# Kernel tuning notes

Measured on AMD Instinct MI355X. Metric: run time of the kernel, lower is better.

## Reference

```python
import jax, jax.numpy as jnp
import numpy as np
import math

N_HEAD = 16
ROPE_BASE = 10000.0


def _rope_cos_sin(seq_len, head_dim, dtype):
    # standard RoPE tables: freqs_i = base^(-2i/d), i in [0, d/2)
    half = head_dim // 2
    inv_freq = ROPE_BASE ** (-(jnp.arange(half, dtype=jnp.float32) * 2.0 / head_dim))
    t = jnp.arange(seq_len, dtype=jnp.float32)
    ang = t[:, None] * inv_freq[None, :]  # [S, d/2]
    return jnp.cos(ang).astype(dtype), jnp.sin(ang).astype(dtype)


def _apply_rope(x, cos, sin):
    # x: [B, S, H, d]; rotate interleaved even/odd pairs
    x1 = x[..., 0::2]
    x2 = x[..., 1::2]
    c = cos[None, :, None, :]
    s = sin[None, :, None, :]
    out = jnp.stack([x1 * c - x2 * s, x1 * s + x2 * c], axis=-1)
    return out.reshape(x.shape)


def setup_inputs() -> dict:
    key = jax.random.key(0)
    kx, kq, kk, kv, ko = jax.random.split(key, 5)
    B, S, H = 2, 2048, 1024
    x = jax.random.normal(kx, (B, S, H), dtype=jnp.float32)
    scale = 0.02
    w_q = jax.random.normal(kq, (H, H), dtype=jnp.float32) * scale
    w_k = jax.random.normal(kk, (H, H), dtype=jnp.float32) * scale
    w_v = jax.random.normal(kv, (H, H), dtype=jnp.float32) * scale
    w_o = jax.random.normal(ko, (H, H), dtype=jnp.float32) * scale
    return {"x": x, "w_q": w_q, "w_k": w_k, "w_v": w_v, "w_o": w_o}


def reference(x, w_q, w_k, w_v, w_o):
    B, S, H = x.shape
    d = H // N_HEAD
    # torch nn.Linear(bias=False): y = x @ W^T, W is [out, in]
    q = (x @ w_q.T).reshape(B, S, N_HEAD, d)
    k = (x @ w_k.T).reshape(B, S, N_HEAD, d)
    v = (x @ w_v.T).reshape(B, S, N_HEAD, d)
    cos, sin = _rope_cos_sin(S, d, x.dtype)
    q = _apply_rope(q, cos, sin)
    k = _apply_rope(k, cos, sin)
    scores = jnp.einsum("bqhd,bkhd->bhqk", q, k) / math.sqrt(d)
    coefs = jax.nn.softmax(scores, axis=-1)
    # NOTE: causal mask is applied AFTER softmax via tril (no renormalization)
    causal = jnp.tril(jnp.ones((S, S), dtype=bool))
    coefs = jnp.where(causal[None, None], coefs, 0.0)
    out = jnp.einsum("bhqk,bkhd->bqhd", coefs, v).reshape(B, S, H)
    return out @ w_o.T
```

## Files before the change

kernel.cpp:

```cpp
#include <hip/hip_runtime.h>
#include <math.h>

#define SEQ   2048
#define HDIM  1024
#define NH    16
#define DH    64
#define MTOT  4096
#define BHTOT 32

typedef _Float16 half_t;
typedef __attribute__((ext_vector_type(2))) __fp16 fp16x2;
typedef __attribute__((ext_vector_type(4))) _Float16 half4;
typedef __attribute__((ext_vector_type(8))) _Float16 half8;
typedef __attribute__((ext_vector_type(4))) float float4v;

typedef __attribute__((address_space(1))) const unsigned int guint;
typedef __attribute__((address_space(3))) unsigned int luint;
__device__ __forceinline__ void glds16(const half_t* g, half_t* l) {
    __builtin_amdgcn_global_load_lds((guint*)g, (luint*)l, 16, 0, 0);
}

__global__ __launch_bounds__(256)
void prep(const float* __restrict__ x,  const float* __restrict__ wq,
          const float* __restrict__ wk, const float* __restrict__ wv,
          const float* __restrict__ wo,
          half_t* __restrict__ xh,  half_t* __restrict__ wqh,
          half_t* __restrict__ wkh, half_t* __restrict__ wvh,
          half_t* __restrict__ woh, float2* __restrict__ rope)
{
    const int bid = blockIdx.x;
    if (bid < 8192) {
        int i = bid * 256 + threadIdx.x;
        const float* s; half_t* d;
        if (i < 1048576) { s = x; d = xh; }
        else {
            int j = i - 1048576;
            int w = j >> 18; i = j & 262143;
            s = (w == 0) ? wq : (w == 1) ? wk : (w == 2) ? wv : wo;
            d = (w == 0) ? wqh : (w == 1) ? wkh : (w == 2) ? wvh : woh;
        }
        float4 v = ((const float4*)s)[i];
        union { half_t h[4]; uint2 u; } tmp;
        tmp.h[0] = (half_t)v.x; tmp.h[1] = (half_t)v.y;
        tmp.h[2] = (half_t)v.z; tmp.h[3] = (half_t)v.w;
        ((uint2*)d)[i] = tmp.u;
    } else {
        int tt = (bid - 8192) * 256 + threadIdx.x;
        int s = tt >> 5, j = tt & 31;
        float inv = powf(10000.0f, -(float)j / 32.0f);
        float ang = (float)s * inv;
        rope[tt] = make_float2(cosf(ang), sinf(ang));
    }
}

__global__ __launch_bounds__(256)
void gemm_qkv(const half_t* __restrict__ A,
              const half_t* __restrict__ w0, const half_t* __restrict__ w1,
              const half_t* __restrict__ w2,
              half_t* __restrict__ Qb, half_t* __restrict__ Kb,
              half_t* __restrict__ Vtb,
              const float2* __restrict__ rope)
{
    const int mode = blockIdx.z;
    const half_t* Bw = (mode == 1) ? w1 : (mode == 2) ? w2 : w0;

    __shared__ __align__(16) half_t Tsh[2][128][64];
    half_t (*Ash)[64] = Tsh[0];
    half_t (*Bsh)[64] = Tsh[1];

    const int t    = threadIdx.x;
    const int lane = t & 63;
    const int wave = t >> 6;
    const int quad = lane >> 4;
    const int l16  = lane & 15;
    const int wr   = (wave >> 1) * 64;
    const int wc   = (wave & 1) * 64;
    const int bm   = blockIdx.x, bn = blockIdx.y;

    const int srow   = lane >> 3;
    const int schunk = (lane & 7) ^ srow;
    const half_t* Asrc = A  + (size_t)(bm * 128 + srow) * HDIM + schunk * 8;
    const half_t* Bsrc = Bw + (size_t)(bn * 128 + srow) * HDIM + schunk * 8;
    const int swz = (l16 & 7) << 4;

    float4v acc[4][4] = {};

    for (int kt = 0; kt < HDIM / 64; ++kt) {
        const half_t* Ak = Asrc + kt * 64;
        const half_t* Bk = Bsrc + kt * 64;
#pragma unroll
        for (int c = 0; c < 4; ++c) {
            const int r8 = wave * 32 + c * 8;
            glds16(Ak + (size_t)r8 * HDIM, &Ash[r8][0]);
            glds16(Bk + (size_t)r8 * HDIM, &Bsh[r8][0]);
        }
        __syncthreads();
#pragma unroll
        for (int kk = 0; kk < 2; ++kk) {
            const int cb = ((quad << 4) | (kk << 6)) ^ swz;
            half8 af[4], bf[4];
#pragma unroll
            for (int mb = 0; mb < 4; ++mb)
                af[mb] = *(const half8*)((const char*)&Ash[wr + mb * 16 + l16][0] + cb);
#pragma unroll
            for (int nb = 0; nb < 4; ++nb)
                bf[nb] = *(const half8*)((const char*)&Bsh[wc + nb * 16 + l16][0] + cb);
#pragma unroll
            for (int mb = 0; mb < 4; ++mb)
#pragma unroll
                for (int nb = 0; nb < 4; ++nb)
                    acc[mb][nb] = __builtin_amdgcn_mfma_f32_16x16x32_f16(af[mb], bf[nb], acc[mb][nb], 0, 0, 0);
        }
        __syncthreads();
    }

    if (mode == 2) {
#pragma unroll
        for (int mb = 0; mb < 4; ++mb)
#pragma unroll
            for (int nb = 0; nb < 4; ++nb) {
                int row0 = bm * 128 + wr + mb * 16 + quad * 4;
                int col  = bn * 128 + wc + nb * 16 + l16;
                int b = row0 >> 11, s0 = row0 & 2047;
                int h = col >> 6,  dd = col & 63;
                union { half_t h4[4]; uint2 u; } tmp;
#pragma unroll
                for (int r = 0; r < 4; ++r) tmp.h4[r] = (half_t)acc[mb][nb][r];
                *(uint2*)&Vtb[((size_t)((b * NH + h) * DH + dd)) * SEQ + s0] = tmp.u;
            }
        return;
    }
    {
        half_t* Ob = (mode == 0) ? Qb : Kb;
        const float scl = (mode == 0) ? 0.125f * 1.44269504088896f : 1.0f;
        const int h = (bn * 128 + wc) >> 6;
        float* E = (float*)&Tsh[0][0][0] + wave * 1088;
#pragma unroll
        for (int mb = 0; mb < 4; ++mb) {
#pragma unroll
            for (int nb = 0; nb < 4; ++nb)
#pragma unroll
                for (int r = 0; r < 4; ++r)
                    E[(quad * 4 + r) * 68 + nb * 16 + l16] = acc[mb][nb][r];
            __asm__ volatile("s_waitcnt lgkmcnt(0)" ::: "memory");
#pragma unroll
            for (int c = 0; c < 2; ++c) {
                const int uidx = c * 64 + lane;
                const int row = uidx >> 3, ch = uidx & 7;
                const int sg = bm * 128 + wr + mb * 16 + row;
                const int b = sg >> 11, s = sg & 2047;
                const float* Er = E + row * 68 + ch * 8;
                const float4 e0 = *(const float4*)Er;
                const float4 e1 = *(const float4*)(Er + 4);
                const float4* rp = (const float4*)(rope + (size_t)s * 32 + ch * 4);
                const float4 r01 = rp[0];
                const float4 r23 = rp[1];
                union { half_t hh[8]; uint4 u; } o;
                o.hh[0] = (half_t)((e0.x * r01.x - e0.y * r01.y) * scl);
                o.hh[1] = (half_t)((e0.x * r01.y + e0.y * r01.x) * scl);
                o.hh[2] = (half_t)((e0.z * r01.z - e0.w * r01.w) * scl);
                o.hh[3] = (half_t)((e0.z * r01.w + e0.w * r01.z) * scl);
                o.hh[4] = (half_t)((e1.x * r23.x - e1.y * r23.y) * scl);
                o.hh[5] = (half_t)((e1.x * r23.y + e1.y * r23.x) * scl);
                o.hh[6] = (half_t)((e1.z * r23.z - e1.w * r23.w) * scl);
                o.hh[7] = (half_t)((e1.z * r23.w + e1.w * r23.z) * scl);
                *(uint4*)&Ob[((size_t)((b * NH + h) * SEQ + s)) * DH + ch * 8] = o.u;
            }
        }
    }
}

__global__ __launch_bounds__(256)
void gemm_out(const half_t* __restrict__ A, const half_t* __restrict__ W,
              float* __restrict__ outF)
{
    __shared__ __align__(16) half_t Ash[64][64];
    __shared__ __align__(16) half_t Bsh[128][64];

    const int t    = threadIdx.x;
    const int lane = t & 63;
    const int wave = t >> 6;
    const int quad = lane >> 4;
    const int l16  = lane & 15;
    const int wr   = (wave >> 1) * 32;
    const int wc   = (wave & 1) * 64;
    const int bm   = blockIdx.x, bn = blockIdx.y;

    const int srow   = lane >> 3;
    const int schunk = (lane & 7) ^ srow;
    const half_t* Asrc = A + (size_t)(bm * 64  + srow) * HDIM + schunk * 8;
    const half_t* Bsrc = W + (size_t)(bn * 128 + srow) * HDIM + schunk * 8;
    const int swz = (l16 & 7) << 4;

    float4v acc[2][4] = {};

    for (int kt = 0; kt < HDIM / 64; ++kt) {
        const half_t* Ak = Asrc + kt * 64;
        const half_t* Bk = Bsrc + kt * 64;
#pragma unroll
        for (int c = 0; c < 2; ++c) {
            const int r8 = wave * 16 + c * 8;
            glds16(Ak + (size_t)r8 * HDIM, &Ash[r8][0]);
        }
#pragma unroll
        for (int c = 0; c < 4; ++c) {
            const int r8 = wave * 32 + c * 8;
            glds16(Bk + (size_t)r8 * HDIM, &Bsh[r8][0]);
        }
        __syncthreads();
#pragma unroll
        for (int kk = 0; kk < 2; ++kk) {
            const int cb = ((quad << 4) | (kk << 6)) ^ swz;
            half8 af[2], bf[4];
#pragma unroll
            for (int mb = 0; mb < 2; ++mb)
                af[mb] = *(const half8*)((const char*)&Ash[wr + mb * 16 + l16][0] + cb);
#pragma unroll
            for (int nb = 0; nb < 4; ++nb)
                bf[nb] = *(const half8*)((const char*)&Bsh[wc + nb * 16 + l16][0] + cb);
#pragma unroll
            for (int mb = 0; mb < 2; ++mb)
#pragma unroll
                for (int nb = 0; nb < 4; ++nb)
                    acc[mb][nb] = __builtin_amdgcn_mfma_f32_16x16x32_f16(af[mb], bf[nb], acc[mb][nb], 0, 0, 0);
        }
        __syncthreads();
    }

#pragma unroll
    for (int mb = 0; mb < 2; ++mb)
#pragma unroll
        for (int nb = 0; nb < 4; ++nb) {
            int row0 = bm * 64 + wr + mb * 16 + quad * 4;
            int col  = bn * 128 + wc + nb * 16 + l16;
#pragma unroll
            for (int r = 0; r < 4; ++r)
                outF[(size_t)(row0 + r) * HDIM + col] = acc[mb][nb][r];
        }
}

__global__ __launch_bounds__(512)
void attn_fused(const half_t* __restrict__ Qb, const half_t* __restrict__ Kb,
                const half_t* __restrict__ Vtb, half_t* __restrict__ AOut)
{
    const int jb = blockIdx.x;
    const int bh = blockIdx.y;

    __shared__ __align__(16) half_t Ksh[2][64][64];
    __shared__ __align__(16) half_t Vsh[2][64][72];

    const int t = threadIdx.x;
    const int wave = t >> 6, lane = t & 63, quad = lane >> 4, l16 = lane & 15;
    const int unit = wave >> 2, wl = wave & 3;
    const int qtile = unit ? (15 - jb) : jb;
    const int q0 = qtile * 128 + wl * 32;
    const int ktop = 2 * (15 - jb) + 1;

    half8 qf[2][2];
#pragma unroll
    for (int g = 0; g < 2; ++g) {
        const half_t* Qp = Qb + ((size_t)bh * SEQ + q0 + g * 16 + l16) * DH + quad * 8;
        qf[g][0] = *(const half8*)Qp;
        qf[g][1] = *(const half8*)(Qp + 32);
    }

    float4v o[2][4] = {};
    float lsum[2] = {0.f, 0.f};

    const int krow = lane >> 3, kpos = lane & 7;
    const int kchunk = kpos ^ krow;
    const half_t* Ksrc0 = Kb + ((size_t)bh * SEQ + wl * 16     + krow) * DH + kchunk * 8;
    const half_t* Ksrc1 = Kb + ((size_t)bh * SEQ + wl * 16 + 8 + krow) * DH + kchunk * 8;
    const int ko1 = ((quad ^ (l16 & 7)) * 8);
    const int ko2 = ko1 ^ 32;

    const int tv  = t & 255;
    const int sr  = tv >> 2;
    const int scc = (tv & 3) * 16;
    const half_t* Vg = Vtb + ((size_t)bh * DH + sr) * SEQ + scc;

    if (unit == 0) {
        glds16(Ksrc0, &Ksh[0][wl * 16][0]);
        glds16(Ksrc1, &Ksh[0][wl * 16 + 8][0]);
    } else {
        *(uint4*)&Vsh[0][sr][scc]     = *(const uint4*)(Vg);
        *(uint4*)&Vsh[0][sr][scc + 8] = *(const uint4*)(Vg + 8);
    }
    __syncthreads();

    for (int kt = 0; kt < SEQ / 64; ++kt) {
        const int cur = kt & 1, nxt = cur ^ 1;
        const bool have_next = (kt + 1 < SEQ / 64);
        const bool next_v    = (kt + 1 <= ktop);

        uint4 va, vb;
        if (unit == 0) {
            if (have_next) {
                const half_t* Kn = Ksrc0 + (size_t)(kt + 1) * 64 * DH;
                glds16(Kn,          &Ksh[nxt][wl * 16][0]);
                glds16(Kn + 8 * DH, &Ksh[nxt][wl * 16 + 8][0]);
            }
        } else if (have_next && next_v) {
            const half_t* Vgk = Vg + (kt + 1) * 64;
            va = *(const uint4*)(Vgk);
            vb = *(const uint4*)(Vgk + 8);
        }

        float4v sc[2][4];
        __builtin_amdgcn_s_setprio(1);
#pragma unroll
        for (int nb = 0; nb < 4; ++nb) {
            const half_t* kp = &Ksh[cur][nb * 16 + l16][0];
            half8 kf0 = *(const half8*)(kp + ko1);
            half8 kf1 = *(const half8*)(kp + ko2);
#pragma unroll
            for (int g = 0; g < 2; ++g) {
                float4v a = {};
                a = __builtin_amdgcn_mfma_f32_16x16x32_f16(kf0, qf[g][0], a, 0, 0, 0);
                a = __builtin_amdgcn_mfma_f32_16x16x32_f16(kf1, qf[g][1], a, 0, 0, 0);
                sc[g][nb] = a;
            }
        }
        __builtin_amdgcn_s_setprio(0);

#pragma unroll
        for (int g = 0; g < 2; ++g)
#pragma unroll
            for (int nb = 0; nb < 4; ++nb)
#pragma unroll
                for (int r = 0; r < 4; ++r) {
                    float e = __builtin_amdgcn_exp2f(sc[g][nb][r]);
                    sc[g][nb][r] = e;
                    lsum[g] += e;
                }

        const int kbase = kt * 64;
        if (kbase <= q0 + 31) {
            if (kbase + 63 > q0) {
#pragma unroll
                for (int g = 0; g < 2; ++g) {
                    int qg = q0 + g * 16 + l16;
#pragma unroll
                    for (int nb = 0; nb < 4; ++nb)
#pragma unroll
                        for (int r = 0; r < 4; ++r)
                            if (kbase + nb * 16 + quad * 4 + r > qg) sc[g][nb][r] = 0.f;
                }
            }
            half4 pf[2][4];
#pragma unroll
            for (int g = 0; g < 2; ++g)
#pragma unroll
                for (int nb = 0; nb < 4; ++nb) {
                    union { fp16x2 v2[2]; half4 v4; } u;
                    u.v2[0] = __builtin_amdgcn_cvt_pkrtz(sc[g][nb][0], sc[g][nb][1]);
                    u.v2[1] = __builtin_amdgcn_cvt_pkrtz(sc[g][nb][2], sc[g][nb][3]);
                    pf[g][nb] = u.v4;
                }
            __builtin_amdgcn_s_setprio(1);
#pragma unroll
            for (int md = 0; md < 4; ++md)
#pragma unroll
                for (int nb = 0; nb < 4; ++nb) {
                    half4 vf = *(const half4*)&Vsh[cur][md * 16 + l16][nb * 16 + quad * 4];
                    o[0][md] = __builtin_amdgcn_mfma_f32_16x16x16f16(vf, pf[0][nb], o[0][md], 0, 0, 0);
                    o[1][md] = __builtin_amdgcn_mfma_f32_16x16x16f16(vf, pf[1][nb], o[1][md], 0, 0, 0);
                }
            __builtin_amdgcn_s_setprio(0);
        }

        if (unit == 1 && have_next && next_v) {
            *(uint4*)&Vsh[nxt][sr][scc]     = va;
            *(uint4*)&Vsh[nxt][sr][scc + 8] = vb;
        }
        __syncthreads();
    }

    const int b = bh >> 4, h = bh & 15;
    const int orow = lane >> 2, occ = (lane & 3) * 16;
    half_t* scr = unit ? ((half_t*)Vsh + wl * 1152) : ((half_t*)Ksh + wl * 1152);
    half_t (*Osh)[72] = (half_t(*)[72])scr;
#pragma unroll
    for (int g = 0; g < 2; ++g) {
        float rs = lsum[g];
        rs += __shfl_xor(rs, 16, 64);
        rs += __shfl_xor(rs, 32, 64);
        const float inv = 1.0f / rs;
#pragma unroll
        for (int md = 0; md < 4; ++md)
#pragma unroll
            for (int r = 0; r < 4; ++r)
                Osh[l16][md * 16 + quad * 4 + r] = (half_t)(o[g][md][r] * inv);
        __asm__ volatile("s_waitcnt lgkmcnt(0)" ::: "memory");
        uint4 o0 = *(const uint4*)&Osh[orow][occ];
        uint4 o1 = *(const uint4*)&Osh[orow][occ + 8];
        const int s = q0 + g * 16 + orow;
        half_t* dst = AOut + ((size_t)(b * SEQ + s)) * HDIM + h * DH + occ;
        *(uint4*)dst       = o0;
        *(uint4*)(dst + 8) = o1;
    }
}

extern "C" void kernel_launch(void* const* d_in, const int* in_sizes, int n_in,
                              void* d_out, int out_size, void* d_ws, size_t ws_size,
                              hipStream_t stream)
{
    const float* x  = (const float*)d_in[0];
    const float* wq = (const float*)d_in[1];
    const float* wk = (const float*)d_in[2];
    const float* wv = (const float*)d_in[3];
    const float* wo = (const float*)d_in[4];
    float* out = (float*)d_out;

    char* ws = (char*)d_ws;
    size_t off = 0;
    auto alloc = [&](size_t bytes) -> void* {
        void* p = ws + off;
        off += (bytes + 255) & ~(size_t)255;
        return p;
    };
    half_t* xh   = (half_t*)alloc((size_t)MTOT * HDIM * 2);
    half_t* wqh  = (half_t*)alloc((size_t)HDIM * HDIM * 2);
    half_t* wkh  = (half_t*)alloc((size_t)HDIM * HDIM * 2);
    half_t* wvh  = (half_t*)alloc((size_t)HDIM * HDIM * 2);
    half_t* woh  = (half_t*)alloc((size_t)HDIM * HDIM * 2);
    half_t* Qb   = (half_t*)alloc((size_t)BHTOT * SEQ * DH * 2);
    half_t* Kb   = (half_t*)alloc((size_t)BHTOT * SEQ * DH * 2);
    half_t* Vtb  = (half_t*)alloc((size_t)BHTOT * SEQ * DH * 2);
    half_t* ah   = (half_t*)alloc((size_t)MTOT * HDIM * 2);
    float2* rope = (float2*)alloc((size_t)SEQ * 32 * sizeof(float2));

    prep<<<8448, 256, 0, stream>>>(x, wq, wk, wv, wo, xh, wqh, wkh, wvh, woh, rope);

    gemm_qkv<<<dim3(32, 8, 3), 256, 0, stream>>>(xh, wqh, wkh, wvh,
                                                 Qb, Kb, Vtb, rope);
    attn_fused<<<dim3(8, 32), 512, 0, stream>>>(Qb, Kb, Vtb, ah);
    gemm_out<<<dim3(64, 8), 256, 0, stream>>>(ah, woh, out);
}
```

Before: 190.2 us.

## Split attention blocks into 256-thread halves pairing low and high query tiles per wave

The attention kernel now launches twice as many 256-thread blocks. Each wave handles one 16-row query group from a low tile and one from the mirrored high tile, so causal work is balanced inside each wave rather than across two 4-wave units. Every thread now loads both K and V, and the P·V MFMAs for the low tile are skipped once it is past its causal limit. The row-sum accumulator is split per register lane to shorten the dependency chain. The goal is more blocks for occupancy and less idle work, at the cost of more K/V reloads per query row overall.

After: 197.2 us. 1.04x slower.

```diff
diff --git a/kernel.cpp b/kernel.cpp
--- a/kernel.cpp
+++ b/kernel.cpp
@@ -239,11 +239,13 @@
         }
 }
 
-__global__ __launch_bounds__(512)
+__global__ __launch_bounds__(256)
 void attn_fused(const half_t* __restrict__ Qb, const half_t* __restrict__ Kb,
                 const half_t* __restrict__ Vtb, half_t* __restrict__ AOut)
 {
-    const int jb = blockIdx.x;
+    const int bx = blockIdx.x;
+    const int p  = bx >> 1;
+    const int hf = bx & 1;
     const int bh = blockIdx.y;
 
     __shared__ __align__(16) half_t Ksh[2][64][64];
@@ -251,41 +253,36 @@
 
     const int t = threadIdx.x;
     const int wave = t >> 6, lane = t & 63, quad = lane >> 4, l16 = lane & 15;
-    const int unit = wave >> 2, wl = wave & 3;
-    const int qtile = unit ? (15 - jb) : jb;
-    const int q0 = qtile * 128 + wl * 32;
-    const int ktop = 2 * (15 - jb) + 1;
+
+    const int q0g[2] = { p * 128 + hf * 64 + wave * 16,
+                         (15 - p) * 128 + hf * 64 + wave * 16 };
+    const int ktop = 2 * (15 - p) + hf;
 
     half8 qf[2][2];
 #pragma unroll
     for (int g = 0; g < 2; ++g) {
-        const half_t* Qp = Qb + ((size_t)bh * SEQ + q0 + g * 16 + l16) * DH + quad * 8;
+        const half_t* Qp = Qb + ((size_t)bh * SEQ + q0g[g] + l16) * DH + quad * 8;
         qf[g][0] = *(const half8*)Qp;
         qf[g][1] = *(const half8*)(Qp + 32);
     }
 
     float4v o[2][4] = {};
-    float lsum[2] = {0.f, 0.f};
+    float4v ls[2] = {};
 
     const int krow = lane >> 3, kpos = lane & 7;
     const int kchunk = kpos ^ krow;
-    const half_t* Ksrc0 = Kb + ((size_t)bh * SEQ + wl * 16     + krow) * DH + kchunk * 8;
-    const half_t* Ksrc1 = Kb + ((size_t)bh * SEQ + wl * 16 + 8 + krow) * DH + kchunk * 8;
+    const half_t* Ksrc = Kb + ((size_t)bh * SEQ + wave * 16 + krow) * DH + kchunk * 8;
     const int ko1 = ((quad ^ (l16 & 7)) * 8);
     const int ko2 = ko1 ^ 32;
 
-    const int tv  = t & 255;
-    const int sr  = tv >> 2;
-    const int scc = (tv & 3) * 16;
+    const int sr  = t >> 2;
+    const int scc = (t & 3) * 16;
     const half_t* Vg = Vtb + ((size_t)bh * DH + sr) * SEQ + scc;
 
-    if (unit == 0) {
-        glds16(Ksrc0, &Ksh[0][wl * 16][0]);
-        glds16(Ksrc1, &Ksh[0][wl * 16 + 8][0]);
-    } else {
-        *(uint4*)&Vsh[0][sr][scc]     = *(const uint4*)(Vg);
-        *(uint4*)&Vsh[0][sr][scc + 8] = *(const uint4*)(Vg + 8);
-    }
+    glds16(Ksrc,          &Ksh[0][wave * 16][0]);
+    glds16(Ksrc + 8 * DH, &Ksh[0][wave * 16 + 8][0]);
+    *(uint4*)&Vsh[0][sr][scc]     = *(const uint4*)(Vg);
+    *(uint4*)&Vsh[0][sr][scc + 8] = *(const uint4*)(Vg + 8);
     __syncthreads();
 
     for (int kt = 0; kt < SEQ / 64; ++kt) {
@@ -293,14 +290,13 @@
         const bool have_next = (kt + 1 < SEQ / 64);
         const bool next_v    = (kt + 1 <= ktop);
 
+        if (have_next) {
+            const half_t* Kn = Ksrc + (size_t)(kt + 1) * 64 * DH;
+            glds16(Kn,          &Ksh[nxt][wave * 16][0]);
+            glds16(Kn + 8 * DH, &Ksh[nxt][wave * 16 + 8][0]);
+        }
         uint4 va, vb;
-        if (unit == 0) {
-            if (have_next) {
-                const half_t* Kn = Ksrc0 + (size_t)(kt + 1) * 64 * DH;
-                glds16(Kn,          &Ksh[nxt][wl * 16][0]);
-                glds16(Kn + 8 * DH, &Ksh[nxt][wl * 16 + 8][0]);
-            }
-        } else if (have_next && next_v) {
+        if (have_next && next_v) {
             const half_t* Vgk = Vg + (kt + 1) * 64;
             va = *(const uint4*)(Vgk);
             vb = *(const uint4*)(Vgk + 8);
@@ -331,45 +327,69 @@
                 for (int r = 0; r < 4; ++r) {
                     float e = __builtin_amdgcn_exp2f(sc[g][nb][r]);
                     sc[g][nb][r] = e;
-                    lsum[g] += e;
+                    ls[g][r] += e;
                 }
 
         const int kbase = kt * 64;
-        if (kbase <= q0 + 31) {
-            if (kbase + 63 > q0) {
-#pragma unroll
-                for (int g = 0; g < 2; ++g) {
-                    int qg = q0 + g * 16 + l16;
-#pragma unroll
-                    for (int nb = 0; nb < 4; ++nb)
-#pragma unroll
-                        for (int r = 0; r < 4; ++r)
-                            if (kbase + nb * 16 + quad * 4 + r > qg) sc[g][nb][r] = 0.f;
-                }
-            }
-            half4 pf[2][4];
-#pragma unroll
-            for (int g = 0; g < 2; ++g)
+        const bool act1 = (kbase <= q0g[1] + 15);
+        const bool act0 = (kbase <= q0g[0] + 15);
+        if (act1) {
+            if (kbase + 63 > q0g[1]) {
+                int qg = q0g[1] + l16;
+#pragma unroll
+                for (int nb = 0; nb < 4; ++nb)
+#pragma unroll
+                    for (int r = 0; r < 4; ++r)
+                        if (kbase + nb * 16 + quad * 4 + r > qg) sc[1][nb][r] = 0.f;
+            }
+            if (act0 && kbase + 63 > q0g[0]) {
+                int qg = q0g[0] + l16;
+#pragma unroll
+                for (int nb = 0; nb < 4; ++nb)
+#pragma unroll
+                    for (int r = 0; r < 4; ++r)
+                        if (kbase + nb * 16 + quad * 4 + r > qg) sc[0][nb][r] = 0.f;
+            }
+            half4 pf1[4], pf0[4];
+#pragma unroll
+            for (int nb = 0; nb < 4; ++nb) {
+                union { fp16x2 v2[2]; half4 v4; } u;
+                u.v2[0] = __builtin_amdgcn_cvt_pkrtz(sc[1][nb][0], sc[1][nb][1]);
+                u.v2[1] = __builtin_amdgcn_cvt_pkrtz(sc[1][nb][2], sc[1][nb][3]);
+                pf1[nb] = u.v4;
+            }
+            if (act0) {
 #pragma unroll
                 for (int nb = 0; nb < 4; ++nb) {
                     union { fp16x2 v2[2]; half4 v4; } u;
-                    u.v2[0] = __builtin_amdgcn_cvt_pkrtz(sc[g][nb][0], sc[g][nb][1]);
-                    u.v2[1] = __builtin_amdgcn_cvt_pkrtz(sc[g][nb][2], sc[g][nb][3]);
-                    pf[g][nb] = u.v4;
+                    u.v2[0] = __builtin_amdgcn_cvt_pkrtz(sc[0][nb][0], sc[0][nb][1]);
+                    u.v2[1] = __builtin_amdgcn_cvt_pkrtz(sc[0][nb][2], sc[0][nb][3]);
+                    pf0[nb] = u.v4;
                 }
+            }
             __builtin_amdgcn_s_setprio(1);
-#pragma unroll
-            for (int md = 0; md < 4; ++md)
-#pragma unroll
-                for (int nb = 0; nb < 4; ++nb) {
-                    half4 vf = *(const half4*)&Vsh[cur][md * 16 + l16][nb * 16 + quad * 4];
-                    o[0][md] = __builtin_amdgcn_mfma_f32_16x16x16f16(vf, pf[0][nb], o[0][md], 0, 0, 0);
-                    o[1][md] = __builtin_amdgcn_mfma_f32_16x16x16f16(vf, pf[1][nb], o[1][md], 0, 0, 0);
-                }
+            if (act0) {
+#pragma unroll
+                for (int md = 0; md < 4; ++md)
+#pragma unroll
+                    for (int nb = 0; nb < 4; ++nb) {
+                        half4 vf = *(const half4*)&Vsh[cur][md * 16 + l16][nb * 16 + quad * 4];
+                        o[1][md] = __builtin_amdgcn_mfma_f32_16x16x16f16(vf, pf1[nb], o[1][md], 0, 0, 0);
+                        o[0][md] = __builtin_amdgcn_mfma_f32_16x16x16f16(vf, pf0[nb], o[0][md], 0, 0, 0);
+                    }
+            } else {
+#pragma unroll
+                for (int md = 0; md < 4; ++md)
+#pragma unroll
+                    for (int nb = 0; nb < 4; ++nb) {
+                        half4 vf = *(const half4*)&Vsh[cur][md * 16 + l16][nb * 16 + quad * 4];
+                        o[1][md] = __builtin_amdgcn_mfma_f32_16x16x16f16(vf, pf1[nb], o[1][md], 0, 0, 0);
+                    }
+            }
             __builtin_amdgcn_s_setprio(0);
         }
 
-        if (unit == 1 && have_next && next_v) {
+        if (have_next && next_v) {
             *(uint4*)&Vsh[nxt][sr][scc]     = va;
             *(uint4*)&Vsh[nxt][sr][scc + 8] = vb;
         }
@@ -378,11 +398,11 @@
 
     const int b = bh >> 4, h = bh & 15;
     const int orow = lane >> 2, occ = (lane & 3) * 16;
-    half_t* scr = unit ? ((half_t*)Vsh + wl * 1152) : ((half_t*)Ksh + wl * 1152);
+    half_t* scr = (half_t*)Ksh + wave * 1152;
     half_t (*Osh)[72] = (half_t(*)[72])scr;
 #pragma unroll
     for (int g = 0; g < 2; ++g) {
-        float rs = lsum[g];
+        float rs = (ls[g][0] + ls[g][1]) + (ls[g][2] + ls[g][3]);
         rs += __shfl_xor(rs, 16, 64);
         rs += __shfl_xor(rs, 32, 64);
         const float inv = 1.0f / rs;
@@ -394,7 +414,7 @@
         __asm__ volatile("s_waitcnt lgkmcnt(0)" ::: "memory");
         uint4 o0 = *(const uint4*)&Osh[orow][occ];
         uint4 o1 = *(const uint4*)&Osh[orow][occ + 8];
-        const int s = q0 + g * 16 + orow;
+        const int s = q0g[g] + orow;
         half_t* dst = AOut + ((size_t)(b * SEQ + s)) * HDIM + h * DH + occ;
         *(uint4*)dst       = o0;
         *(uint4*)(dst + 8) = o1;
@@ -434,6 +454,6 @@
 
     gemm_qkv<<<dim3(32, 8, 3), 256, 0, stream>>>(xh, wqh, wkh, wvh,
                                                  Qb, Kb, Vtb, rope);
-    attn_fused<<<dim3(8, 32), 512, 0, stream>>>(Qb, Kb, Vtb, ah);
+    attn_fused<<<dim3(16, 32), 256, 0, stream>>>(Qb, Kb, Vtb, ah);
     gemm_out<<<dim3(64, 8), 256, 0, stream>>>(ah, woh, out);
 }
```

## Split attention query work across twice as many blocks with one 16-row group per wave

Applied to the files above, without the earlier changes.

Each attention block now covers half as many query rows: every wave handles a single 16-row query group instead of two, and the grid doubles from 8 to 16 blocks per head. All waves share K and V tile loading (each thread loads one chunk) instead of splitting the K and V loads between the two wave groups. The launch bound now asks for 4 blocks per CU, so per-thread registers shrink and more blocks can be resident. The cost is that K/V tiles are loaded from global memory twice as often in total, and each wave gets less MFMA work per LDS read.

New measurement: 189.0 us. No clear change (-0.6%).

```diff
diff --git a/kernel.cpp b/kernel.cpp
--- a/kernel.cpp
+++ b/kernel.cpp
@@ -239,11 +239,13 @@
         }
 }
 
-__global__ __launch_bounds__(512)
+__global__ __launch_bounds__(512, 4)
 void attn_fused(const half_t* __restrict__ Qb, const half_t* __restrict__ Kb,
                 const half_t* __restrict__ Vtb, half_t* __restrict__ AOut)
 {
-    const int jb = blockIdx.x;
+    const int bx = blockIdx.x;
+    const int p  = bx >> 1;
+    const int hf = bx & 1;
     const int bh = blockIdx.y;
 
     __shared__ __align__(16) half_t Ksh[2][64][64];
@@ -251,41 +253,30 @@
 
     const int t = threadIdx.x;
     const int wave = t >> 6, lane = t & 63, quad = lane >> 4, l16 = lane & 15;
-    const int unit = wave >> 2, wl = wave & 3;
-    const int qtile = unit ? (15 - jb) : jb;
-    const int q0 = qtile * 128 + wl * 32;
-    const int ktop = 2 * (15 - jb) + 1;
-
-    half8 qf[2][2];
-#pragma unroll
-    for (int g = 0; g < 2; ++g) {
-        const half_t* Qp = Qb + ((size_t)bh * SEQ + q0 + g * 16 + l16) * DH + quad * 8;
-        qf[g][0] = *(const half8*)Qp;
-        qf[g][1] = *(const half8*)(Qp + 32);
-    }
-
-    float4v o[2][4] = {};
-    float lsum[2] = {0.f, 0.f};
+    const int heavy = wave >> 2, wl = wave & 3;
+    const int qtile = heavy ? (15 - p) : p;
+    const int q0 = qtile * 128 + hf * 64 + wl * 16;
+    const int ktop = 2 * (15 - p) + hf;
+
+    const half_t* Qp = Qb + ((size_t)bh * SEQ + q0 + l16) * DH + quad * 8;
+    const half8 qf0 = *(const half8*)Qp;
+    const half8 qf1 = *(const half8*)(Qp + 32);
+
+    float4v o[4] = {};
+    float4v ls = {};
 
     const int krow = lane >> 3, kpos = lane & 7;
     const int kchunk = kpos ^ krow;
-    const half_t* Ksrc0 = Kb + ((size_t)bh * SEQ + wl * 16     + krow) * DH + kchunk * 8;
-    const half_t* Ksrc1 = Kb + ((size_t)bh * SEQ + wl * 16 + 8 + krow) * DH + kchunk * 8;
+    const half_t* Ksrc = Kb + ((size_t)bh * SEQ + wave * 8 + krow) * DH + kchunk * 8;
     const int ko1 = ((quad ^ (l16 & 7)) * 8);
     const int ko2 = ko1 ^ 32;
 
-    const int tv  = t & 255;
-    const int sr  = tv >> 2;
-    const int scc = (tv & 3) * 16;
+    const int sr  = t >> 3;
+    const int scc = (t & 7) * 8;
     const half_t* Vg = Vtb + ((size_t)bh * DH + sr) * SEQ + scc;
 
-    if (unit == 0) {
-        glds16(Ksrc0, &Ksh[0][wl * 16][0]);
-        glds16(Ksrc1, &Ksh[0][wl * 16 + 8][0]);
-    } else {
-        *(uint4*)&Vsh[0][sr][scc]     = *(const uint4*)(Vg);
-        *(uint4*)&Vsh[0][sr][scc + 8] = *(const uint4*)(Vg + 8);
-    }
+    glds16(Ksrc, &Ksh[0][wave * 8][0]);
+    *(uint4*)&Vsh[0][sr][scc] = *(const uint4*)(Vg);
     __syncthreads();
 
     for (int kt = 0; kt < SEQ / 64; ++kt) {
@@ -293,96 +284,75 @@
         const bool have_next = (kt + 1 < SEQ / 64);
         const bool next_v    = (kt + 1 <= ktop);
 
-        uint4 va, vb;
-        if (unit == 0) {
-            if (have_next) {
-                const half_t* Kn = Ksrc0 + (size_t)(kt + 1) * 64 * DH;
-                glds16(Kn,          &Ksh[nxt][wl * 16][0]);
-                glds16(Kn + 8 * DH, &Ksh[nxt][wl * 16 + 8][0]);
-            }
-        } else if (have_next && next_v) {
-            const half_t* Vgk = Vg + (kt + 1) * 64;
-            va = *(const uint4*)(Vgk);
-            vb = *(const uint4*)(Vgk + 8);
-        }
-
-        float4v sc[2][4];
+        if (have_next)
+            glds16(Ksrc + (size_t)(kt + 1) * 64 * DH, &Ksh[nxt][wave * 8][0]);
+        uint4 va;
+        if (have_next && next_v)
+            va = *(const uint4*)(Vg + (kt + 1) * 64);
+
+        float4v sc[4];
         __builtin_amdgcn_s_setprio(1);
 #pragma unroll
         for (int nb = 0; nb < 4; ++nb) {
             const half_t* kp = &Ksh[cur][nb * 16 + l16][0];
             half8 kf0 = *(const half8*)(kp + ko1);
             half8 kf1 = *(const half8*)(kp + ko2);
-#pragma unroll
-            for (int g = 0; g < 2; ++g) {
-                float4v a = {};
-                a = __builtin_amdgcn_mfma_f32_16x16x32_f16(kf0, qf[g][0], a, 0, 0, 0);
-                a = __builtin_amdgcn_mfma_f32_16x16x32_f16(kf1, qf[g][1], a, 0, 0, 0);
-                sc[g][nb] = a;
+            float4v a = {};
+            a = __builtin_amdgcn_mfma_f32_16x16x32_f16(kf0, qf0, a, 0, 0, 0);
+            a = __builtin_amdgcn_mfma_f32_16x16x32_f16(kf1, qf1, a, 0, 0, 0);
+            sc[nb] = a;
+        }
+        __builtin_amdgcn_s_setprio(0);
+
+#pragma unroll
+        for (int nb = 0; nb < 4; ++nb)
+#pragma unroll
+            for (int r = 0; r < 4; ++r) {
+                float e = __builtin_amdgcn_exp2f(sc[nb][r]);
+                sc[nb][r] = e;
+                ls[r] += e;
             }
-        }
-        __builtin_amdgcn_s_setprio(0);
-
-#pragma unroll
-        for (int g = 0; g < 2; ++g)
-#pragma unroll
-            for (int nb = 0; nb < 4; ++nb)
-#pragma unroll
-                for (int r = 0; r < 4; ++r) {
-                    float e = __builtin_amdgcn_exp2f(sc[g][nb][r]);
-                    sc[g][nb][r] = e;
-                    lsum[g] += e;
-                }
 
         const int kbase = kt * 64;
-        if (kbase <= q0 + 31) {
+        if (kbase <= q0 + 15) {
             if (kbase + 63 > q0) {
-#pragma unroll
-                for (int g = 0; g < 2; ++g) {
-                    int qg = q0 + g * 16 + l16;
-#pragma unroll
-                    for (int nb = 0; nb < 4; ++nb)
-#pragma unroll
-                        for (int r = 0; r < 4; ++r)
-                            if (kbase + nb * 16 + quad * 4 + r > qg) sc[g][nb][r] = 0.f;
-                }
+                int qg = q0 + l16;
+#pragma unroll
+                for (int nb = 0; nb < 4; ++nb)
+#pragma unroll
+                    for (int r = 0; r < 4; ++r)
+                        if (kbase + nb * 16 + quad * 4 + r > qg) sc[nb][r] = 0.f;
             }
-            half4 pf[2][4];
-#pragma unroll
-            for (int g = 0; g < 2; ++g)
-#pragma unroll
-                for (int nb = 0; nb < 4; ++nb) {
-                    union { fp16x2 v2[2]; half4 v4; } u;
-                    u.v2[0] = __builtin_amdgcn_cvt_pkrtz(sc[g][nb][0], sc[g][nb][1]);
-                    u.v2[1] = __builtin_amdgcn_cvt_pkrtz(sc[g][nb][2], sc[g][nb][3]);
-                    pf[g][nb] = u.v4;
-                }
+            half4 pf[4];
+#pragma unroll
+            for (int nb = 0; nb < 4; ++nb) {
+                union { fp16x2 v2[2]; half4 v4; } u;
+                u.v2[0] = __builtin_amdgcn_cvt_pkrtz(sc[nb][0], sc[nb][1]);
+                u.v2[1] = __builtin_amdgcn_cvt_pkrtz(sc[nb][2], sc[nb][3]);
+                pf[nb] = u.v4;
+            }
             __builtin_amdgcn_s_setprio(1);
 #pragma unroll
             for (int md = 0; md < 4; ++md)
 #pragma unroll
                 for (int nb = 0; nb < 4; ++nb) {
                     half4 vf = *(const half4*)&Vsh[cur][md * 16 + l16][nb * 16 + quad * 4];
-                    o[0][md] = __builtin_amdgcn_mfma_f32_16x16x16f16(vf, pf[0][nb], o[0][md], 0, 0, 0);
-                    o[1][md] = __builtin_amdgcn_mfma_f32_16x16x16f16(vf, pf[1][nb], o[1][md], 0, 0, 0);
+                    o[md] = __builtin_amdgcn_mfma_f32_16x16x16f16(vf, pf[nb], o[md], 0, 0, 0);
                 }
             __builtin_amdgcn_s_setprio(0);
         }
 
-        if (unit == 1 && have_next && next_v) {
-            *(uint4*)&Vsh[nxt][sr][scc]     = va;
-            *(uint4*)&Vsh[nxt][sr][scc + 8] = vb;
-        }
+        if (have_next && next_v)
+            *(uint4*)&Vsh[nxt][sr][scc] = va;
         __syncthreads();
     }
 
     const int b = bh >> 4, h = bh & 15;
     const int orow = lane >> 2, occ = (lane & 3) * 16;
-    half_t* scr = unit ? ((half_t*)Vsh + wl * 1152) : ((half_t*)Ksh + wl * 1152);
+    half_t* scr = (heavy ? (half_t*)Vsh : (half_t*)Ksh) + wl * 1152;
     half_t (*Osh)[72] = (half_t(*)[72])scr;
-#pragma unroll
-    for (int g = 0; g < 2; ++g) {
-        float rs = lsum[g];
+    {
+        float rs = (ls[0] + ls[1]) + (ls[2] + ls[3]);
         rs += __shfl_xor(rs, 16, 64);
         rs += __shfl_xor(rs, 32, 64);
         const float inv = 1.0f / rs;
@@ -390,11 +360,11 @@
         for (int md = 0; md < 4; ++md)
 #pragma unroll
             for (int r = 0; r < 4; ++r)
-                Osh[l16][md * 16 + quad * 4 + r] = (half_t)(o[g][md][r] * inv);
+                Osh[l16][md * 16 + quad * 4 + r] = (half_t)(o[md][r] * inv);
         __asm__ volatile("s_waitcnt lgkmcnt(0)" ::: "memory");
         uint4 o0 = *(const uint4*)&Osh[orow][occ];
         uint4 o1 = *(const uint4*)&Osh[orow][occ + 8];
-        const int s = q0 + g * 16 + orow;
+        const int s = q0 + orow;
         half_t* dst = AOut + ((size_t)(b * SEQ + s)) * HDIM + h * DH + occ;
         *(uint4*)dst       = o0;
         *(uint4*)(dst + 8) = o1;
@@ -434,6 +404,6 @@
 
     gemm_qkv<<<dim3(32, 8, 3), 256, 0, stream>>>(xh, wqh, wkh, wvh,
                                                  Qb, Kb, Vtb, rope);
-    attn_fused<<<dim3(8, 32), 512, 0, stream>>>(Qb, Kb, Vtb, ah);
+    attn_fused<<<dim3(16, 32), 512, 0, stream>>>(Qb, Kb, Vtb, ah);
     gemm_out<<<dim3(64, 8), 256, 0, stream>>>(ah, woh, out);
 }
```
